# Performance work log

Hardware: AMD Instinct MI355X
Metric: run time of the kernel (lower is better)

## Reference

```python
import jax, jax.numpy as jnp
import numpy as np

KERNEL_SIZE = 21
SIGMA = 3.0


def _gaussian_kernel_2d(kernel_size, sigma, dtype):
    ax = jnp.arange(kernel_size, dtype=dtype) - (kernel_size - 1) / 2.0
    xx, yy = jnp.meshgrid(ax, ax, indexing='ij')
    k = jnp.exp(-(xx ** 2 + yy ** 2) / (2.0 * sigma ** 2))
    return k / jnp.sum(k)


def setup_inputs() -> dict:
    key = jax.random.key(0)
    x = jax.random.normal(key, (32, 3, 512, 512), dtype=jnp.float32)
    return {"x": x}


def reference(x):
    B, C, H, W = x.shape
    k2d = _gaussian_kernel_2d(KERNEL_SIZE, SIGMA, x.dtype)  # [K, K]
    # depthwise weights: OIHW with feature_group_count=C -> [C, 1, K, K]
    w = jnp.broadcast_to(k2d[None, None], (C, 1, KERNEL_SIZE, KERNEL_SIZE))
    pad = KERNEL_SIZE // 2
    x_pad = jnp.pad(x, ((0, 0), (0, 0), (pad, pad), (pad, pad)), mode='reflect')
    y = jax.lax.conv_general_dilated(
        x_pad, w,
        window_strides=(1, 1),
        padding='VALID',
        dimension_numbers=('NCHW', 'OIHW', 'NCHW'),
        feature_group_count=C,
    )
    return y
```

## Files before the change

### kernel.cpp

```cpp
#include <hip/hip_runtime.h>

#define HH  512
#define WW  512
#define RAD 10
#define KK  21
#define SEG 64

__global__ __launch_bounds__(256) void gauss_blur_kernel(
    const float* __restrict__ x, float* __restrict__ out)
{
    const float w[KK] = {
        0.00051432f, 0.00147793f, 0.00380033f, 0.00874446f, 0.01800488f,
        0.03317359f, 0.05469399f, 0.08069227f, 0.10652936f, 0.12584957f,
        0.13303907f,
        0.12584957f, 0.10652936f, 0.08069227f, 0.05469399f, 0.03317359f,
        0.01800488f, 0.00874446f, 0.00380033f, 0.00147793f, 0.00051432f
    };

    __shared__ __align__(16) float vbuf[2][536];

    const int t   = threadIdx.x;
    const int c0  = 2 * t;
    const int c1  = c0 + 1;
    const int seg = blockIdx.x;
    const int img = blockIdx.y;
    const int y0  = seg * SEG;

    const float* xim = x   + (size_t)img * (HH * WW);
    float*       oim = out + (size_t)img * (HH * WW);

    auto loadrow = [&](int r) -> float2 {
        int rr = r < 0 ? -r : (r > HH - 1 ? 2 * (HH - 1) - r : r);
        return *(const float2*)(xim + rr * WW + c0);
    };

    float2 hist[KK];

    #pragma unroll
    for (int i = 0; i < KK - 1; ++i)
        hist[i] = loadrow(y0 - RAD + i);

    float2 nxt = loadrow(y0 + RAD);

    for (int i2 = 0; i2 < SEG; ++i2) {
        const int y = y0 + i2;
        hist[KK - 1] = nxt;
        nxt = loadrow(y + RAD + 1);

        float vx = 0.f, vy = 0.f;
        #pragma unroll
        for (int k = 0; k < KK; ++k) {
            vx += w[k] * hist[k].x;
            vy += w[k] * hist[k].y;
        }

        float* vb = vbuf[i2 & 1];
        *(float2*)(vb + RAD + c0) = make_float2(vx, vy);
        if (c0 >= 1 && c0 <= RAD) vb[RAD - c0] = vx;
        if (c1 <= RAD)            vb[RAD - c1] = vy;
        if (c0 >= WW - 11 && c0 <= WW - 2) vb[RAD + 2 * (WW - 1) - c0] = vx;
        if (c1 >= WW - 11 && c1 <= WW - 2) vb[RAD + 2 * (WW - 1) - c1] = vy;

        __syncthreads();

        const float* vr = vb + c0;
        float wn[KK + 1];
        #pragma unroll
        for (int j = 0; j < 11; ++j) {
            float2 t2 = *(const float2*)(vr + 2 * j);
            wn[2 * j]     = t2.x;
            wn[2 * j + 1] = t2.y;
        }
        float acc0 = 0.f, acc1 = 0.f;
        #pragma unroll
        for (int j = 0; j < KK; ++j) {
            acc0 += w[j] * wn[j];
            acc1 += w[j] * wn[j + 1];
        }
        *(float2*)(oim + (size_t)y * WW + c0) = make_float2(acc0, acc1);

        #pragma unroll
        for (int i = 0; i < KK - 1; ++i)
            hist[i] = hist[i + 1];
    }
}

extern "C" void kernel_launch(void* const* d_in, const int* in_sizes, int n_in,
                              void* d_out, int out_size, void* d_ws, size_t ws_size,
                              hipStream_t stream) {
    const float* x = (const float*)d_in[0];
    float* out = (float*)d_out;
    const int n_img = in_sizes[0] / (HH * WW);
    dim3 grid(HH / SEG, n_img);
    gauss_blur_kernel<<<grid, dim3(256), 0, stream>>>(x, out);
}
```

Baseline: 205.4 us.

## Batch vertical pass into shared tile, compute 16-wide horizontal outputs per thread

The vertical pass now fills a 16-row shared-memory tile before a single barrier, replacing the per-row double-buffered sync. The horizontal pass is remapped so each thread computes 16 consecutive outputs from a 36-element float4-loaded window, which reduces LDS reads per output and allows float4 stores. Segment height drops to 16 rows, giving more blocks, and launch bounds request 4 blocks per SM. The cost is more vertical halo reloads per segment (36 input rows for 16 outputs), more shared memory, and higher register pressure.

```diff
diff --git a/kernel.cpp b/kernel.cpp
--- a/kernel.cpp
+++ b/kernel.cpp
@@ -4,12 +4,13 @@
 #define WW  512
 #define RAD 10
 #define KK  21
-#define SEG 64
+#define SEG 16
+#define LSTRIDE 540
 
-__global__ __launch_bounds__(256) void gauss_blur_kernel(
+__global__ __launch_bounds__(256, 4) void gauss_blur_kernel(
     const float* __restrict__ x, float* __restrict__ out)
 {
-    const float w[KK] = {
+    const float wt[KK] = {
         0.00051432f, 0.00147793f, 0.00380033f, 0.00874446f, 0.01800488f,
         0.03317359f, 0.05469399f, 0.08069227f, 0.10652936f, 0.12584957f,
         0.13303907f,
@@ -17,14 +18,13 @@
         0.01800488f, 0.00874446f, 0.00380033f, 0.00147793f, 0.00051432f
     };
 
-    __shared__ __align__(16) float vbuf[2][536];
+    __shared__ __align__(16) float vbuf[SEG * LSTRIDE];
 
     const int t   = threadIdx.x;
     const int c0  = 2 * t;
     const int c1  = c0 + 1;
-    const int seg = blockIdx.x;
+    const int y0  = blockIdx.x * SEG;
     const int img = blockIdx.y;
-    const int y0  = seg * SEG;
 
     const float* xim = x   + (size_t)img * (HH * WW);
     float*       oim = out + (size_t)img * (HH * WW);
@@ -35,53 +35,64 @@
     };
 
     float2 hist[KK];
+    #pragma unroll
+    for (int i = 0; i < KK; ++i)
+        hist[i] = loadrow(y0 - RAD + i);
 
     #pragma unroll
-    for (int i = 0; i < KK - 1; ++i)
-        hist[i] = loadrow(y0 - RAD + i);
-
-    float2 nxt = loadrow(y0 + RAD);
-
-    for (int i2 = 0; i2 < SEG; ++i2) {
-        const int y = y0 + i2;
-        hist[KK - 1] = nxt;
-        nxt = loadrow(y + RAD + 1);
-
+    for (int r = 0; r < SEG; ++r) {
         float vx = 0.f, vy = 0.f;
         #pragma unroll
         for (int k = 0; k < KK; ++k) {
-            vx += w[k] * hist[k].x;
-            vy += w[k] * hist[k].y;
+            vx += wt[k] * hist[k].x;
+            vy += wt[k] * hist[k].y;
+        }
+        float* vb = vbuf + r * LSTRIDE;
+        *(float2*)(vb + RAD + c0) = make_float2(vx, vy);
+        if (c0 >= 1 && c0 <= RAD)           vb[RAD - c0] = vx;
+        if (c1 <= RAD)                      vb[RAD - c1] = vy;
+        if (c0 >= WW - 11 && c0 <= WW - 2)  vb[RAD + 2 * (WW - 1) - c0] = vx;
+        if (c1 >= WW - 11 && c1 <= WW - 2)  vb[RAD + 2 * (WW - 1) - c1] = vy;
+
+        if (r < SEG - 1) {
+            #pragma unroll
+            for (int i = 0; i < KK - 1; ++i) hist[i] = hist[i + 1];
+            hist[KK - 1] = loadrow(y0 + r + 1 + RAD);
+        }
+    }
+
+    __syncthreads();
+
+    #pragma unroll
+    for (int task = 0; task < 2; ++task) {
+        const int tid = t + task * 256;
+        const int r   = tid & (SEG - 1);
+        const int q   = tid >> 4;
+        const float* vr = vbuf + r * LSTRIDE + q * 16;
+
+        float wnd[36];
+        #pragma unroll
+        for (int j = 0; j < 9; ++j) {
+            float4 v4 = *(const float4*)(vr + 4 * j);
+            wnd[4*j]   = v4.x; wnd[4*j+1] = v4.y;
+            wnd[4*j+2] = v4.z; wnd[4*j+3] = v4.w;
         }
 
-        float* vb = vbuf[i2 & 1];
-        *(float2*)(vb + RAD + c0) = make_float2(vx, vy);
-        if (c0 >= 1 && c0 <= RAD) vb[RAD - c0] = vx;
-        if (c1 <= RAD)            vb[RAD - c1] = vy;
-        if (c0 >= WW - 11 && c0 <= WW - 2) vb[RAD + 2 * (WW - 1) - c0] = vx;
-        if (c1 >= WW - 11 && c1 <= WW - 2) vb[RAD + 2 * (WW - 1) - c1] = vy;
+        float acc[16];
+        #pragma unroll
+        for (int j = 0; j < 16; ++j) {
+            float s = 0.f;
+            #pragma unroll
+            for (int k = 0; k < KK; ++k)
+                s += wt[k] * wnd[j + k];
+            acc[j] = s;
+        }
 
-        __syncthreads();
-
-        const float* vr = vb + c0;
-        float wn[KK + 1];
+        float* op = oim + (size_t)(y0 + r) * WW + q * 16;
         #pragma unroll
-        for (int j = 0; j < 11; ++j) {
-            float2 t2 = *(const float2*)(vr + 2 * j);
-            wn[2 * j]     = t2.x;
-            wn[2 * j + 1] = t2.y;
-        }
-        float acc0 = 0.f, acc1 = 0.f;
-        #pragma unroll
-        for (int j = 0; j < KK; ++j) {
-            acc0 += w[j] * wn[j];
-            acc1 += w[j] * wn[j + 1];
-        }
-        *(float2*)(oim + (size_t)y * WW + c0) = make_float2(acc0, acc1);
-
-        #pragma unroll
-        for (int i = 0; i < KK - 1; ++i)
-            hist[i] = hist[i + 1];
+        for (int j = 0; j < 4; ++j)
+            *(float4*)(op + 4 * j) =
+                make_float4(acc[4*j], acc[4*j+1], acc[4*j+2], acc[4*j+3]);
     }
 }
 
```

Result: faster. 201.2 us (-2.1%).
